# Optimization experiments

Measured on AMD Instinct MI355X. Metric: run time of the kernel, lower is better.

## Reference

```python
import jax, jax.numpy as jnp
import numpy as np

B = 512; S = 2048; K = 128; E = 64; A = 128; H = 4; DK = A // H; OD = 64; BITS = 32
FOH = 15; FMH = 4; FSP = 4; LSP = 50
VOH = 10001; VMH = 100001; VSP = 10001
D0 = 27 * E


def _short_attn(tgt, seq, mask, qW, qb, kW, kb, vW, vb, oW, ob):
    # tgt [F,b,1,E], seq [F,b,s,E], mask [F,b,1,s] bool
    F_, b_, s_, _ = seq.shape
    q = (jnp.einsum('fbte,fea->fbta', tgt, qW) + qb[:, None, None, :]).reshape(F_, b_, -1, H, DK)
    k = (jnp.einsum('fbse,fea->fbsa', seq, kW) + kb[:, None, None, :]).reshape(F_, b_, s_, H, DK)
    v = (jnp.einsum('fbse,fea->fbsa', seq, vW) + vb[:, None, None, :]).reshape(F_, b_, s_, H, DK)
    scores = jnp.einsum('fbthd,fbshd->fbhts', q, k) / (DK ** 0.5)
    scores = jnp.where(mask[:, :, None, :, :], scores, -jnp.inf)
    attn = jax.nn.softmax(scores, axis=-1)
    out = jnp.einsum('fbhts,fbshd->fbthd', attn, v).reshape(F_, b_, -1, A)
    return jnp.einsum('fbta,fao->fbto', out, oW) + ob[:, None, None, :]  # [F,b,1,OD]


def _forward(one_hot_tables, multi_hot_tables, special_tables, hash_weights,
             sqW, sqb, skW, skb, svW, svb, soW, sob,
             lqW, lqb, lkW, lkb, lvW, lvb, loW, lob,
             W0, b0, W1, b1, W2, b2, outW, outb,
             one_hot_ids, multi_hot_ids, special_ids):
    lookup = jax.vmap(lambda t, i: t[i], in_axes=(0, 0))
    oh_emb = jax.vmap(lambda t, i: t[i], in_axes=(0, 1))(one_hot_tables, one_hot_ids)  # [FOH,B,E]
    mh_mask = multi_hot_ids >= 0                                                       # [FMH,B,S]
    mh_emb = lookup(multi_hot_tables, jnp.where(mh_mask, multi_hot_ids, 0))            # [FMH,B,S,E]
    sp_mask = special_ids >= 0
    sp_emb = (lookup(special_tables, jnp.where(sp_mask, special_ids, 0))
              * sp_mask[..., None].astype(jnp.float32)).sum(axis=2)                    # [FSP,B,E] sum combiner
    tgt = oh_emb[:FMH][:, :, None, :]  # targets = first 4 one-hot fields, [4,B,1,E]
    # short attention over first K candidates of each history
    short = _short_attn(tgt, mh_emb[:, :, :K, :], mh_mask[:, :, None, :K],
                        sqW, sqb, skW, skb, svW, svb, soW, sob)                        # [4,B,1,OD]
    # long attention: LSH hash -> hamming-sim topk -> gather -> attention
    th = (jnp.einsum('fbe,eh->fbh', tgt[:, :, 0, :], hash_weights) > 0).astype(jnp.float32)
    sh = (jnp.einsum('fbse,eh->fbsh', mh_emb, hash_weights) > 0).astype(jnp.float32)
    sim = -jnp.sum(jnp.abs(sh - th[:, :, None, :]), axis=-1)                           # [4,B,S]
    sim = jnp.where(mh_mask, sim, -jnp.inf)
    _, idx = jax.lax.top_k(sim, K)                                                     # [4,B,K]
    topk_seq = jnp.take_along_axis(mh_emb, idx[..., None], axis=2)                     # [4,B,K,E]
    topk_mask = jnp.take_along_axis(mh_mask, idx, axis=2)[:, :, None, :]
    long = _short_attn(tgt, topk_seq, topk_mask,
                       lqW, lqb, lkW, lkb, lvW, lvb, loW, lob)                         # [4,B,1,OD]
    b_ = oh_emb.shape[1]
    feats = jnp.concatenate([
        oh_emb.transpose(1, 0, 2).reshape(b_, -1),
        sp_emb.transpose(1, 0, 2).reshape(b_, -1),
        short[:, :, 0, :].transpose(1, 0, 2).reshape(b_, -1),
        long[:, :, 0, :].transpose(1, 0, 2).reshape(b_, -1)], axis=-1)                 # [B, 27*E]
    x = jax.nn.relu(feats @ W0 + b0)
    x = jax.nn.relu(x @ W1 + b1)
    x = jax.nn.relu(x @ W2 + b2)
    logits = (x @ outW + outb)[:, 0]
    return jax.nn.sigmoid(logits), logits


def setup_inputs():
    ks = list(jax.random.split(jax.random.key(0), 64))
    def nrm(shape, scale):
        return jax.random.normal(ks.pop(), shape, dtype=jnp.float32) * scale
    std = (2.0 / 512.0) ** 0.5
    d = {}
    d['one_hot_tables'] = nrm((FOH, VOH, E), std)
    d['multi_hot_tables'] = nrm((FMH, VMH, E), std)
    d['special_tables'] = nrm((FSP, VSP, E), std)
    d['hash_weights'] = nrm((E, BITS), 1.0)
    for p in ('s', 'l'):
        d[p + 'qW'] = nrm((FMH, E, A), E ** -0.5); d[p + 'qb'] = nrm((FMH, A), 0.01)
        d[p + 'kW'] = nrm((FMH, E, A), E ** -0.5); d[p + 'kb'] = nrm((FMH, A), 0.01)
        d[p + 'vW'] = nrm((FMH, E, A), E ** -0.5); d[p + 'vb'] = nrm((FMH, A), 0.01)
        d[p + 'oW'] = nrm((FMH, A, OD), A ** -0.5); d[p + 'ob'] = nrm((FMH, OD), 0.01)
    dims = [D0, 1024, 512, 256]
    for i in range(3):
        d['W%d' % i] = nrm((dims[i], dims[i + 1]), dims[i] ** -0.5)
        d['b%d' % i] = nrm((dims[i + 1],), 0.01)
    d['outW'] = nrm((256, 1), 256 ** -0.5)
    d['outb'] = nrm((1,), 0.01)
    d['one_hot_ids'] = jax.random.randint(ks.pop(), (B, FOH), 0, VOH, dtype=jnp.int32)
    d['multi_hot_ids'] = jax.random.randint(ks.pop(), (FMH, B, S), 0, VMH, dtype=jnp.int32)
    d['special_ids'] = jax.random.randint(ks.pop(), (FSP, B, LSP), 0, VSP, dtype=jnp.int32)
    return d


def reference(one_hot_tables, multi_hot_tables, special_tables, hash_weights, sqW, sqb, skW, skb, svW, svb, soW, sob, lqW, lqb, lkW, lkb, lvW, lvb, loW, lob, W0, b0, W1, b1, W2, b2, outW, outb, one_hot_ids, multi_hot_ids, special_ids):
    return _forward(one_hot_tables, multi_hot_tables, special_tables, hash_weights,
                    sqW, sqb, skW, skb, svW, svb, soW, sob,
                    lqW, lqb, lkW, lkb, lvW, lvb, loW, lob,
                    W0, b0, W1, b1, W2, b2, outW, outb,
                    one_hot_ids, multi_hot_ids, special_ids)
```

## Files before the change

### kernel.cpp

```cpp
#include <hip/hip_runtime.h>
#include <math.h>

#define F_MH 4
#define NB   512
#define SEQ  2048
#define TOPK 128
#define EDIM 64
#define ADIM 128
#define VOH  10001
#define VMH  100001
#define NROWS (F_MH * VMH)
#define D0   1728
#define RSQRT32 0.17677669529663687f

typedef __bf16 bf16x8 __attribute__((ext_vector_type(8)));
typedef __bf16 bf16x4 __attribute__((ext_vector_type(4)));
typedef float  f32x4  __attribute__((ext_vector_type(4)));

__global__ __launch_bounds__(128) void k_hash(const float* __restrict__ tab,
                                              const float* __restrict__ hw,
                                              unsigned int* __restrict__ sig)
{
    __shared__ float rows[128][65];
    __shared__ float4 hwl[512];
    const int t = threadIdx.x;
#pragma unroll
    for (int i = 0; i < 4; ++i) hwl[t + i * 128] = ((const float4*)hw)[t + i * 128];
    const long long base_dw = (long long)blockIdx.x * 32768;
    const long long lim = (long long)NROWS * 64;
    float4 pf[16];
#pragma unroll
    for (int i = 0; i < 16; ++i) {
        const long long idx = base_dw + i * 512 + t * 4;
        pf[i] = make_float4(0.f, 0.f, 0.f, 0.f);
        if (idx < lim) pf[i] = *(const float4*)(tab + idx);
    }
    for (int c = 0; c < 4; ++c) {
        __syncthreads();
#pragma unroll
        for (int i = 0; i < 16; ++i) {
            const int idx = i * 512 + t * 4;
            const int row = idx >> 6, e = idx & 63;
            rows[row][e + 0] = pf[i].x; rows[row][e + 1] = pf[i].y;
            rows[row][e + 2] = pf[i].z; rows[row][e + 3] = pf[i].w;
        }
        __syncthreads();
        if (c < 3) {
#pragma unroll
            for (int i = 0; i < 16; ++i) {
                const long long idx = base_dw + (long long)(c + 1) * 8192 + i * 512 + t * 4;
                pf[i] = make_float4(0.f, 0.f, 0.f, 0.f);
                if (idx < lim) pf[i] = *(const float4*)(tab + idx);
            }
        }
        float4 acc[8];
#pragma unroll
        for (int h = 0; h < 8; ++h) acc[h] = make_float4(0.f, 0.f, 0.f, 0.f);
#pragma unroll 8
        for (int e = 0; e < 64; ++e) {
            const float x = rows[t][e];
#pragma unroll
            for (int h = 0; h < 8; ++h) {
                const float4 w = hwl[e * 8 + h];
                acc[h].x += x * w.x; acc[h].y += x * w.y;
                acc[h].z += x * w.z; acc[h].w += x * w.w;
            }
        }
        unsigned int bits = 0u;
#pragma unroll
        for (int h = 0; h < 8; ++h) {
            bits |= (acc[h].x > 0.f ? 1u : 0u) << (h * 4);
            bits |= (acc[h].y > 0.f ? 2u : 0u) << (h * 4);
            bits |= (acc[h].z > 0.f ? 4u : 0u) << (h * 4);
            bits |= (acc[h].w > 0.f ? 8u : 0u) << (h * 4);
        }
        const int r = blockIdx.x * 512 + c * 128 + t;
        if (r < NROWS) sig[r] = bits;
    }
}

__global__ __launch_bounds__(256) void k_topk(const float* __restrict__ oh_tab,
                                              const float* __restrict__ hw,
                                              const unsigned int* __restrict__ sig,
                                              const int* __restrict__ oh_ids,
                                              const int* __restrict__ mh_ids,
                                              int* __restrict__ sel)
{
    const int b = blockIdx.x, f = blockIdx.y, t = threadIdx.x;
    __shared__ float tgt[64];
    __shared__ unsigned int thbits;
    __shared__ int hist[34];
    __shared__ int c_lt[256], c_eq[256];
    __shared__ int s_dstar, s_cntlt;
    if (t < 64) tgt[t] = oh_tab[((size_t)f * VOH + oh_ids[b * 15 + f]) * 64 + t];
    if (t == 0) thbits = 0u;
    if (t < 34) hist[t] = 0;
    __syncthreads();
    if (t < 32) {
        float acc = 0.f;
#pragma unroll
        for (int e = 0; e < 64; ++e) acc += tgt[e] * hw[e * 32 + t];
        if (acc > 0.f) atomicOr(&thbits, 1u << t);
    }
    __syncthreads();
    const unsigned int th = thbits;
    const int* idp = mh_ids + (size_t)(f * NB + b) * SEQ + t * 8;
    int ids[8], dv[8];
#pragma unroll
    for (int j = 0; j < 8; ++j) {
        int id = idp[j];
        ids[j] = id;
        int d = (id >= 0) ? __popc(sig[f * VMH + id] ^ th) : 33;
        dv[j] = d;
        atomicAdd(&hist[d], 1);
    }
    __syncthreads();
    if (t == 0) {
        int cum = 0, ds = 33, cl = 0;
        for (int d = 0; d <= 33; ++d) {
            if (cum + hist[d] >= TOPK) { ds = d; cl = cum; break; }
            cum += hist[d];
        }
        s_dstar = ds; s_cntlt = cl;
    }
    __syncthreads();
    const int Dstar = s_dstar, cntlt = s_cntlt;
    int nlt = 0, neq = 0;
#pragma unroll
    for (int j = 0; j < 8; ++j) {
        nlt += (dv[j] < Dstar);
        neq += (dv[j] == Dstar);
    }
    c_lt[t] = nlt; c_eq[t] = neq;
    __syncthreads();
    for (int off = 1; off < 256; off <<= 1) {
        int vl = 0, ve = 0;
        if (t >= off) { vl = c_lt[t - off]; ve = c_eq[t - off]; }
        __syncthreads();
        c_lt[t] += vl; c_eq[t] += ve;
        __syncthreads();
    }
    int lt_pos = c_lt[t] - nlt;
    int eq_pos = cntlt + c_eq[t] - neq;
    int* selp = sel + (size_t)(f * NB + b) * TOPK;
#pragma unroll
    for (int j = 0; j < 8; ++j) {
        if (dv[j] < Dstar) { selp[lt_pos++] = ids[j]; }
        else if (dv[j] == Dstar) {
            if (eq_pos < TOPK) selp[eq_pos] = ids[j];
            eq_pos++;
        }
    }
}

__global__ __launch_bounds__(256) void k_fold(const float* __restrict__ sqW, const float* __restrict__ sqb,
                                              const float* __restrict__ skW,
                                              const float* __restrict__ svW, const float* __restrict__ svb,
                                              const float* __restrict__ soW, const float* __restrict__ sob,
                                              const float* __restrict__ lqW, const float* __restrict__ lqb,
                                              const float* __restrict__ lkW,
                                              const float* __restrict__ lvW, const float* __restrict__ lvb,
                                              const float* __restrict__ loW, const float* __restrict__ lob,
                                              float* __restrict__ Mq, float* __restrict__ B1,
                                              float* __restrict__ VO, float* __restrict__ bvo)
{
    const int f = blockIdx.x, z = blockIdx.y, h = blockIdx.z, t = threadIdx.x;
    const float* WQ = (z ? lqW : sqW) + (size_t)f * 8192;
    const float* bq = (z ? lqb : sqb) + f * 128;
    const float* WK = (z ? lkW : skW) + (size_t)f * 8192;
    const float* WV = (z ? lvW : svW) + (size_t)f * 8192;
    const float* bv = (z ? lvb : svb) + f * 128;
    const float* WO = (z ? loW : soW) + (size_t)f * 8192;
    const float* bo = (z ? lob : sob) + f * 64;

    __shared__ float wq[64][33], wk[64][33], wv[64][33], wo[32][65];
#pragma unroll
    for (int i = 0; i < 8; ++i) {
        int j = t + i * 256;
        wq[j >> 5][j & 31] = WQ[(j >> 5) * 128 + h * 32 + (j & 31)];
        wk[j >> 5][j & 31] = WK[(j >> 5) * 128 + h * 32 + (j & 31)];
        wv[j >> 5][j & 31] = WV[(j >> 5) * 128 + h * 32 + (j & 31)];
        wo[j >> 6][j & 63] = WO[(h * 32 + (j >> 6)) * 64 + (j & 63)];
    }
    __syncthreads();
    const int lane = t & 63, grp = t >> 6;
    float* Mqb = Mq + (size_t)(((z * 4 + f) * 4 + h)) * 4096;
    float* VOb = VO + (size_t)(((z * 4 + f) * 4 + h)) * 4096;
#pragma unroll 4
    for (int g = 0; g < 16; ++g) {
        const int ep = grp * 16 + g;
        float am = 0.f, av = 0.f;
#pragma unroll
        for (int d = 0; d < 32; ++d) {
            am += wq[ep][d] * wk[lane][d];
            av += wv[ep][d] * wo[d][lane];
        }
        Mqb[ep * 64 + lane] = am;
        VOb[ep * 64 + lane] = av;
    }
    if (t < 64) {
        float acc = 0.f;
#pragma unroll
        for (int d = 0; d < 32; ++d) acc += bq[h * 32 + d] * wk[t][d];
        B1[((z * 4 + f) * 4 + h) * 64 + t] = acc;
    }
    if (h == 0 && t >= 64 && t < 128) {
        const int o = t - 64;
        float acc = bo[o];
        for (int a = 0; a < 128; ++a) acc += bv[a] * WO[a * 64 + o];
        bvo[(z * 4 + f) * 64 + o] = acc;
    }
}

__global__ __launch_bounds__(256, 4) void k_attn(const float* __restrict__ oh_tab,
                                                 const float* __restrict__ mh_tab,
                                                 const int* __restrict__ oh_ids,
                                                 const int* __restrict__ mh_ids,
                                                 const int* __restrict__ sel,
                                                 const float* __restrict__ Mq,
                                                 const float* __restrict__ B1,
                                                 const float* __restrict__ VO,
                                                 const float* __restrict__ bvo,
                                                 __bf16* __restrict__ feats)
{
    const int b = blockIdx.x, f = blockIdx.y, z = blockIdx.z, t = threadIdx.x;
    const int zf = z * 4 + f;
    const float* Mqb = Mq + (size_t)zf * 4 * 4096;
    const float* B1b = B1 + zf * 4 * 64;
    const float* VOb = VO + (size_t)zf * 4 * 4096;
    const float* bvob = bvo + zf * 64;

    __shared__ float seq[128][65];
    __shared__ float tgt[64];
    __shared__ int   sid[128];
    __shared__ float qk[4][64];
    __shared__ float sc[4][128];
    __shared__ float wemb[4][64];
    __shared__ float partial[4][64];

    if (t < 64) tgt[t] = oh_tab[((size_t)f * VOH + oh_ids[b * 15 + f]) * 64 + t];
    if (t < 128) {
        int id;
        if (z == 0) id = mh_ids[(size_t)(f * NB + b) * SEQ + t];
        else        id = sel[(size_t)(f * NB + b) * TOPK + t];
        sid[t] = id;
    }
    __syncthreads();
    float4 ev[2];
#pragma unroll
    for (int i = 0; i < 2; ++i) {
        const int v = t + i * 256;
        const int row = v >> 1, c4 = (v & 1) << 5;
        (void)row; (void)c4;
    }
#pragma unroll
    for (int i = 0; i < 2; ++i) {
        const int v = t + i * 256;
        const int row = v >> 2, c4 = (v & 3) << 4;
        (void)row; (void)c4;
    }
    float4 g[8];
#pragma unroll
    for (int i = 0; i < 8; ++i) {
        const int v = t + i * 256;
        const int row = v >> 4, c4 = (v & 15) << 2;
        const int id = sid[row];
        g[i] = make_float4(0.f, 0.f, 0.f, 0.f);
        if (id >= 0) g[i] = *(const float4*)&mh_tab[((size_t)f * VMH + id) * 64 + c4];
    }
    {
        const int h = t >> 6, e = t & 63;
        float acc = B1b[h * 64 + e];
        const float* mrow = Mqb + h * 4096 + e;
#pragma unroll 16
        for (int ep = 0; ep < 64; ++ep) acc += tgt[ep] * mrow[ep * 64];
        qk[h][e] = acc * RSQRT32;
    }
#pragma unroll
    for (int i = 0; i < 8; ++i) {
        const int v = t + i * 256;
        const int row = v >> 4, c4 = (v & 15) << 2;
        seq[row][c4 + 0] = g[i].x; seq[row][c4 + 1] = g[i].y;
        seq[row][c4 + 2] = g[i].z; seq[row][c4 + 3] = g[i].w;
    }
    __syncthreads();
#pragma unroll
    for (int rep = 0; rep < 2; ++rep) {
        const int idx = t + rep * 256;
        const int h = idx >> 7, s = idx & 127;
        float acc = 0.f;
#pragma unroll
        for (int e4 = 0; e4 < 16; ++e4) {
            const float4 q4 = *(const float4*)&qk[h][e4 * 4];
            acc += seq[s][e4 * 4 + 0] * q4.x + seq[s][e4 * 4 + 1] * q4.y
                 + seq[s][e4 * 4 + 2] * q4.z + seq[s][e4 * 4 + 3] * q4.w;
        }
        sc[h][s] = (sid[s] >= 0) ? acc : -INFINITY;
    }
    __syncthreads();
    {
        const int h = t >> 6, l = t & 63;
        float v0 = sc[h][l], v1 = sc[h][l + 64];
        float m = fmaxf(v0, v1);
        for (int off = 32; off; off >>= 1) m = fmaxf(m, __shfl_xor(m, off));
        float p0 = expf(v0 - m), p1 = expf(v1 - m);
        float ssum = p0 + p1;
        for (int off = 32; off; off >>= 1) ssum += __shfl_xor(ssum, off);
        float inv = 1.f / ssum;
        sc[h][l] = p0 * inv; sc[h][l + 64] = p1 * inv;
    }
    {
        const int h = t >> 6, e = t & 63;
        float acc = 0.f;
#pragma unroll 8
        for (int s4 = 0; s4 < 32; ++s4) {
            const float4 a4 = *(const float4*)&sc[h][s4 * 4];
            acc += a4.x * seq[s4 * 4 + 0][e] + a4.y * seq[s4 * 4 + 1][e]
                 + a4.z * seq[s4 * 4 + 2][e] + a4.w * seq[s4 * 4 + 3][e];
        }
        wemb[h][e] = acc;
    }
    {
        const int h = t >> 6, o = t & 63;
        float acc = 0.f;
        const float* vrow = VOb + h * 4096 + o;
#pragma unroll 16
        for (int e = 0; e < 64; ++e) acc += wemb[h][e] * vrow[e * 64];
        partial[h][o] = acc;
    }
    __syncthreads();
    if (t < 64) {
        float acc = partial[0][t] + partial[1][t] + partial[2][t] + partial[3][t] + bvob[t];
        feats[(size_t)b * D0 + (z ? 1472 : 1216) + f * 64 + t] = (__bf16)acc;
    }
}

__global__ __launch_bounds__(256) void k_feats(const float* __restrict__ oh_tab,
                                               const float* __restrict__ sp_tab,
                                               const int* __restrict__ oh_ids,
                                               const int* __restrict__ sp_ids,
                                               __bf16* __restrict__ feats)
{
    const int b = blockIdx.x, t = threadIdx.x;
    __shared__ int sidl[200];
    __shared__ int ohid[15];
    if (t < 200) sidl[t] = sp_ids[(size_t)((t / 50) * NB + b) * 50 + (t % 50)];
    if (t >= 240 && t < 255) ohid[t - 240] = oh_ids[b * 15 + (t - 240)];
    __syncthreads();
    __bf16* fr = feats + (size_t)b * D0;
    for (int p = t; p < 960; p += 256) {
        int f = p >> 6, e = p & 63;
        fr[p] = (__bf16)oh_tab[((size_t)f * VOH + ohid[f]) * 64 + e];
    }
    {
        int f = t >> 6, e = t & 63;
        float acc = 0.f;
        for (int j = 0; j < 50; ++j) {
            int id = sidl[f * 50 + j];
            if (id >= 0) acc += sp_tab[((size_t)f * VOH + id) * 64 + e];
        }
        fr[960 + t] = (__bf16)acc;
    }
}

__global__ __launch_bounds__(256) void k_trans(const float* __restrict__ W,
                                               __bf16* __restrict__ WT,
                                               int K, int N)
{
    __shared__ float tile[32][33];
    const int t = threadIdx.x;
    const int n0 = blockIdx.x * 32, k0 = blockIdx.y * 32;
    const int c = t & 31, r = t >> 5;
#pragma unroll
    for (int i = 0; i < 4; ++i)
        tile[r + 8 * i][c] = W[(size_t)(k0 + r + 8 * i) * N + n0 + c];
    __syncthreads();
#pragma unroll
    for (int i = 0; i < 4; ++i)
        WT[(size_t)(n0 + r + 8 * i) * K + k0 + c] = (__bf16)tile[c][r + 8 * i];
}

__global__ __launch_bounds__(256) void gemm_mfma(const __bf16* __restrict__ A,
                                                 const __bf16* __restrict__ BT,
                                                 const float* __restrict__ bias,
                                                 __bf16* __restrict__ C,
                                                 int M, int N, int K, int relu)
{
    __shared__ __bf16 As[64][72];
    __shared__ __bf16 Bs[64][72];
    const int t = threadIdx.x;
    const int n0 = blockIdx.x * 64, m0 = blockIdx.y * 64;
    const int wave = t >> 6, lane = t & 63;
    const int wm = (wave >> 1) * 32, wn = (wave & 1) * 32;
    const int row16 = lane & 15, quad = lane >> 4;
    f32x4 acc[2][2] = {};
    const int sr = t >> 3;
    const int sseg = (t & 7) * 8;
    for (int k0 = 0; k0 < K; k0 += 64) {
        bf16x8 av0 = *(const bf16x8*)&A[(size_t)(m0 + sr) * K + k0 + sseg];
        bf16x8 av1 = *(const bf16x8*)&A[(size_t)(m0 + sr + 32) * K + k0 + sseg];
        bf16x8 bv0 = *(const bf16x8*)&BT[(size_t)(n0 + sr) * K + k0 + sseg];
        bf16x8 bv1 = *(const bf16x8*)&BT[(size_t)(n0 + sr + 32) * K + k0 + sseg];
        __syncthreads();
        *(bf16x8*)&As[sr][sseg] = av0;
        *(bf16x8*)&As[sr + 32][sseg] = av1;
        *(bf16x8*)&Bs[sr][sseg] = bv0;
        *(bf16x8*)&Bs[sr + 32][sseg] = bv1;
        __syncthreads();
#pragma unroll
        for (int kk = 0; kk < 2; ++kk) {
            bf16x8 a0 = *(const bf16x8*)&As[wm + row16][kk * 32 + quad * 8];
            bf16x8 a1 = *(const bf16x8*)&As[wm + 16 + row16][kk * 32 + quad * 8];
            bf16x8 b0 = *(const bf16x8*)&Bs[wn + row16][kk * 32 + quad * 8];
            bf16x8 b1 = *(const bf16x8*)&Bs[wn + 16 + row16][kk * 32 + quad * 8];
            acc[0][0] = __builtin_amdgcn_mfma_f32_16x16x32_bf16(a0, b0, acc[0][0], 0, 0, 0);
            acc[0][1] = __builtin_amdgcn_mfma_f32_16x16x32_bf16(a0, b1, acc[0][1], 0, 0, 0);
            acc[1][0] = __builtin_amdgcn_mfma_f32_16x16x32_bf16(a1, b0, acc[1][0], 0, 0, 0);
            acc[1][1] = __builtin_amdgcn_mfma_f32_16x16x32_bf16(a1, b1, acc[1][1], 0, 0, 0);
        }
    }
#pragma unroll
    for (int i = 0; i < 2; ++i)
#pragma unroll
        for (int j = 0; j < 2; ++j) {
            const int col = n0 + wn + j * 16 + row16;
            const float bz = bias[col];
#pragma unroll
            for (int r = 0; r < 4; ++r) {
                const int rowm = m0 + wm + i * 16 + quad * 4 + r;
                float v = acc[i][j][r] + bz;
                if (relu) v = fmaxf(v, 0.f);
                C[(size_t)rowm * N + col] = (__bf16)v;
            }
        }
}

__global__ __launch_bounds__(256) void k_out(const __bf16* __restrict__ x2,
                                             const float* __restrict__ outW,
                                             const float* __restrict__ outb,
                                             float* __restrict__ out)
{
    const int t = threadIdx.x;
    const int wave = t >> 6, lane = t & 63;
    const int row = blockIdx.x * 4 + wave;
    bf16x4 xv = *(const bf16x4*)&x2[(size_t)row * 256 + lane * 4];
    const float4 wv = *(const float4*)&outW[lane * 4];
    float v = (float)xv[0] * wv.x + (float)xv[1] * wv.y
            + (float)xv[2] * wv.z + (float)xv[3] * wv.w;
    for (int off = 32; off; off >>= 1) v += __shfl_down(v, off);
    if (lane == 0) {
        float lg = v + outb[0];
        out[row] = 1.f / (1.f + expf(-lg));
        out[NB + row] = lg;
    }
}

extern "C" void kernel_launch(void* const* d_in, const int* in_sizes, int n_in,
                              void* d_out, int out_size, void* d_ws, size_t ws_size,
                              hipStream_t stream)
{
    const float* oh_tab = (const float*)d_in[0];
    const float* mh_tab = (const float*)d_in[1];
    const float* sp_tab = (const float*)d_in[2];
    const float* hw     = (const float*)d_in[3];
    const float* sqW = (const float*)d_in[4];  const float* sqb = (const float*)d_in[5];
    const float* skW = (const float*)d_in[6];  const float* skb = (const float*)d_in[7];
    const float* svW = (const float*)d_in[8];  const float* svb = (const float*)d_in[9];
    const float* soW = (const float*)d_in[10]; const float* sob = (const float*)d_in[11];
    const float* lqW = (const float*)d_in[12]; const float* lqb = (const float*)d_in[13];
    const float* lkW = (const float*)d_in[14]; const float* lkb = (const float*)d_in[15];
    const float* lvW = (const float*)d_in[16]; const float* lvb = (const float*)d_in[17];
    const float* loW = (const float*)d_in[18]; const float* lob = (const float*)d_in[19];
    const float* W0 = (const float*)d_in[20];  const float* b0 = (const float*)d_in[21];
    const float* W1 = (const float*)d_in[22];  const float* b1 = (const float*)d_in[23];
    const float* W2 = (const float*)d_in[24];  const float* b2 = (const float*)d_in[25];
    const float* outW = (const float*)d_in[26]; const float* outb = (const float*)d_in[27];
    const int* oh_ids = (const int*)d_in[28];
    const int* mh_ids = (const int*)d_in[29];
    const int* sp_ids = (const int*)d_in[30];
    (void)skb; (void)lkb;

    char* ws = (char*)d_ws;
    unsigned int* sig = (unsigned int*)(ws + 0);
    int*    sel   = (int*)   (ws + 1600512);
    __bf16* feats = (__bf16*)(ws + 2649088);
    __bf16* x0    = (__bf16*)(ws + 4418560);
    __bf16* x1    = (__bf16*)(ws + 5467136);
    __bf16* x2    = (__bf16*)(ws + 5991424);
    __bf16* WT0   = (__bf16*)(ws + 6253568);
    __bf16* WT1   = (__bf16*)(ws + 9792512);
    __bf16* WT2   = (__bf16*)(ws + 10841088);
    float*  Mq    = (float*) (ws + 11103232);
    float*  VO    = (float*) (ws + 11627520);
    float*  B1    = (float*) (ws + 12151808);
    float*  bvo   = (float*) (ws + 12160000);

    k_trans<<<dim3(1024 / 32, 1728 / 32), 256, 0, stream>>>(W0, WT0, 1728, 1024);
    k_trans<<<dim3(512 / 32, 1024 / 32), 256, 0, stream>>>(W1, WT1, 1024, 512);
    k_trans<<<dim3(256 / 32, 512 / 32), 256, 0, stream>>>(W2, WT2, 512, 256);
    k_fold<<<dim3(F_MH, 2, 4), 256, 0, stream>>>(sqW, sqb, skW, svW, svb, soW, sob,
                                                 lqW, lqb, lkW, lvW, lvb, loW, lob,
                                                 Mq, B1, VO, bvo);

    k_hash<<<(NROWS + 511) / 512, 128, 0, stream>>>(mh_tab, hw, sig);
    k_topk<<<dim3(NB, F_MH), 256, 0, stream>>>(oh_tab, hw, sig, oh_ids, mh_ids, sel);
    k_feats<<<NB, 256, 0, stream>>>(oh_tab, sp_tab, oh_ids, sp_ids, feats);
    k_attn<<<dim3(NB, F_MH, 2), 256, 0, stream>>>(oh_tab, mh_tab, oh_ids, mh_ids, sel,
                                                  Mq, B1, VO, bvo, feats);
    gemm_mfma<<<dim3(16, 8), 256, 0, stream>>>(feats, WT0, b0, x0, 512, 1024, 1728, 1);
    gemm_mfma<<<dim3(8, 8), 256, 0, stream>>>(x0, WT1, b1, x1, 512, 512, 1024, 1);
    gemm_mfma<<<dim3(4, 8), 256, 0, stream>>>(x1, WT2, b2, x2, 512, 256, 512, 1);
    k_out<<<NB / 4, 256, 0, stream>>>(x2, outW, outb, (float*)d_out);
}
```

Baseline: 484.6 us.

## Compute LSH hash signatures with split-bf16 MFMA instead of scalar FMA

The hashing kernel that projects every multi-hot table row onto 32 hyperplanes now uses 16x16x32 bf16 MFMA instructions in place of per-thread scalar FMA loops. To stay close to fp32 accuracy, inputs and weights are each split into high and low bf16 parts and three MFMAs are accumulated. Sign bits are packed with wave ballots, and the block grows to 256 threads with vectorized LDS stores. The split-bf16 product still differs slightly from fp32, so signs of values very near zero may flip and change which top-k candidates are selected. Some unused dead loops are also removed from the attention kernel.

After: 418.9 us. 13.6% less time.

```diff
diff --git a/kernel.cpp b/kernel.cpp
--- a/kernel.cpp
+++ b/kernel.cpp
@@ -17,65 +17,94 @@
 typedef __bf16 bf16x4 __attribute__((ext_vector_type(4)));
 typedef float  f32x4  __attribute__((ext_vector_type(4)));
 
-__global__ __launch_bounds__(128) void k_hash(const float* __restrict__ tab,
+__global__ __launch_bounds__(256) void k_hash(const float* __restrict__ tab,
                                               const float* __restrict__ hw,
                                               unsigned int* __restrict__ sig)
 {
-    __shared__ float rows[128][65];
-    __shared__ float4 hwl[512];
+    __shared__ float rows[128][68];
     const int t = threadIdx.x;
-#pragma unroll
-    for (int i = 0; i < 4; ++i) hwl[t + i * 128] = ((const float4*)hw)[t + i * 128];
+    const int lane = t & 63, wave = t >> 6;
+    const int m = lane & 15, quad = lane >> 4;
+
+    bf16x8 whf[2][2], wlf[2][2];
+#pragma unroll
+    for (int ks = 0; ks < 2; ++ks)
+#pragma unroll
+        for (int hf = 0; hf < 2; ++hf) {
+            bf16x8 bh, bl;
+#pragma unroll
+            for (int j = 0; j < 8; ++j) {
+                const float w = hw[(ks * 32 + quad * 8 + j) * 32 + hf * 16 + m];
+                const __bf16 h = (__bf16)w;
+                bh[j] = h;
+                bl[j] = (__bf16)(w - (float)h);
+            }
+            whf[ks][hf] = bh; wlf[ks][hf] = bl;
+        }
+
     const long long base_dw = (long long)blockIdx.x * 32768;
     const long long lim = (long long)NROWS * 64;
-    float4 pf[16];
-#pragma unroll
-    for (int i = 0; i < 16; ++i) {
-        const long long idx = base_dw + i * 512 + t * 4;
+    float4 pf[8];
+#pragma unroll
+    for (int i = 0; i < 8; ++i) {
+        const long long idx = base_dw + i * 1024 + t * 4;
         pf[i] = make_float4(0.f, 0.f, 0.f, 0.f);
         if (idx < lim) pf[i] = *(const float4*)(tab + idx);
     }
     for (int c = 0; c < 4; ++c) {
         __syncthreads();
 #pragma unroll
-        for (int i = 0; i < 16; ++i) {
-            const int idx = i * 512 + t * 4;
-            const int row = idx >> 6, e = idx & 63;
-            rows[row][e + 0] = pf[i].x; rows[row][e + 1] = pf[i].y;
-            rows[row][e + 2] = pf[i].z; rows[row][e + 3] = pf[i].w;
+        for (int i = 0; i < 8; ++i) {
+            const int v = t + i * 256;
+            *(float4*)&rows[v >> 4][(v & 15) << 2] = pf[i];
         }
         __syncthreads();
         if (c < 3) {
 #pragma unroll
-            for (int i = 0; i < 16; ++i) {
-                const long long idx = base_dw + (long long)(c + 1) * 8192 + i * 512 + t * 4;
+            for (int i = 0; i < 8; ++i) {
+                const long long idx = base_dw + (long long)(c + 1) * 8192 + i * 1024 + t * 4;
                 pf[i] = make_float4(0.f, 0.f, 0.f, 0.f);
                 if (idx < lim) pf[i] = *(const float4*)(tab + idx);
             }
         }
-        float4 acc[8];
-#pragma unroll
-        for (int h = 0; h < 8; ++h) acc[h] = make_float4(0.f, 0.f, 0.f, 0.f);
-#pragma unroll 8
-        for (int e = 0; e < 64; ++e) {
-            const float x = rows[t][e];
-#pragma unroll
-            for (int h = 0; h < 8; ++h) {
-                const float4 w = hwl[e * 8 + h];
-                acc[h].x += x * w.x; acc[h].y += x * w.y;
-                acc[h].z += x * w.z; acc[h].w += x * w.w;
+#pragma unroll
+        for (int tile = 0; tile < 2; ++tile) {
+            const int rbase = wave * 32 + tile * 16;
+            f32x4 acc0 = {0.f, 0.f, 0.f, 0.f}, acc1 = {0.f, 0.f, 0.f, 0.f};
+#pragma unroll
+            for (int ks = 0; ks < 2; ++ks) {
+                const float* src = &rows[rbase + m][ks * 32 + quad * 8];
+                const float4 x0 = *(const float4*)(src);
+                const float4 x1 = *(const float4*)(src + 4);
+                float xs[8] = {x0.x, x0.y, x0.z, x0.w, x1.x, x1.y, x1.z, x1.w};
+                bf16x8 ah, al;
+#pragma unroll
+                for (int j = 0; j < 8; ++j) {
+                    const __bf16 hx = (__bf16)xs[j];
+                    ah[j] = hx;
+                    al[j] = (__bf16)(xs[j] - (float)hx);
+                }
+                acc0 = __builtin_amdgcn_mfma_f32_16x16x32_bf16(ah, whf[ks][0], acc0, 0, 0, 0);
+                acc0 = __builtin_amdgcn_mfma_f32_16x16x32_bf16(ah, wlf[ks][0], acc0, 0, 0, 0);
+                acc0 = __builtin_amdgcn_mfma_f32_16x16x32_bf16(al, whf[ks][0], acc0, 0, 0, 0);
+                acc1 = __builtin_amdgcn_mfma_f32_16x16x32_bf16(ah, whf[ks][1], acc1, 0, 0, 0);
+                acc1 = __builtin_amdgcn_mfma_f32_16x16x32_bf16(ah, wlf[ks][1], acc1, 0, 0, 0);
+                acc1 = __builtin_amdgcn_mfma_f32_16x16x32_bf16(al, whf[ks][1], acc1, 0, 0, 0);
             }
-        }
-        unsigned int bits = 0u;
-#pragma unroll
-        for (int h = 0; h < 8; ++h) {
-            bits |= (acc[h].x > 0.f ? 1u : 0u) << (h * 4);
-            bits |= (acc[h].y > 0.f ? 2u : 0u) << (h * 4);
-            bits |= (acc[h].z > 0.f ? 4u : 0u) << (h * 4);
-            bits |= (acc[h].w > 0.f ? 8u : 0u) << (h * 4);
-        }
-        const int r = blockIdx.x * 512 + c * 128 + t;
-        if (r < NROWS) sig[r] = bits;
+#pragma unroll
+            for (int j = 0; j < 4; ++j) {
+                const unsigned long long m0 = __ballot(acc0[j] > 0.f);
+                const unsigned long long m1 = __ballot(acc1[j] > 0.f);
+                if (m == 0) {
+                    const unsigned int bits =
+                        (unsigned int)((m0 >> (quad * 16)) & 0xFFFFull) |
+                        ((unsigned int)((m1 >> (quad * 16)) & 0xFFFFull) << 16);
+                    const long long gr = (long long)blockIdx.x * 512 + c * 128
+                                       + rbase + quad * 4 + j;
+                    if (gr < NROWS) sig[gr] = bits;
+                }
+            }
+        }
     }
 }
 
@@ -246,19 +275,6 @@
         sid[t] = id;
     }
     __syncthreads();
-    float4 ev[2];
-#pragma unroll
-    for (int i = 0; i < 2; ++i) {
-        const int v = t + i * 256;
-        const int row = v >> 1, c4 = (v & 1) << 5;
-        (void)row; (void)c4;
-    }
-#pragma unroll
-    for (int i = 0; i < 2; ++i) {
-        const int v = t + i * 256;
-        const int row = v >> 2, c4 = (v & 3) << 4;
-        (void)row; (void)c4;
-    }
     float4 g[8];
 #pragma unroll
     for (int i = 0; i < 8; ++i) {
@@ -502,7 +518,7 @@
                                                  lqW, lqb, lkW, lvW, lvb, loW, lob,
                                                  Mq, B1, VO, bvo);
 
-    k_hash<<<(NROWS + 511) / 512, 128, 0, stream>>>(mh_tab, hw, sig);
+    k_hash<<<(NROWS + 511) / 512, 256, 0, stream>>>(mh_tab, hw, sig);
     k_topk<<<dim3(NB, F_MH), 256, 0, stream>>>(oh_tab, hw, sig, oh_ids, mh_ids, sel);
     k_feats<<<NB, 256, 0, stream>>>(oh_tab, sp_tab, oh_ids, sp_ids, feats);
     k_attn<<<dim3(NB, F_MH, 2), 256, 0, stream>>>(oh_tab, mh_tab, oh_ids, mh_ids, sel,
```
